# Performance work log

Hardware: AMD Instinct MI355X
Metric: run time of the kernel (lower is better)

The kernel has to match this reference:

```python
import jax, jax.numpy as jnp
import numpy as np

LEAK = 0.2

def _leaky(h):
    return jnp.where(h >= 0, h, LEAK * h)

def setup_inputs() -> dict:
    key = jax.random.key(0)
    ks = jax.random.split(key, 12)
    B, C, H, W = 4, 19, 256, 512
    ndf = 64
    dims = [C, ndf, ndf * 2, ndf * 4, ndf * 8, 1]  # 19->64->128->256->512->1
    inp = {
        "x": jax.random.normal(ks[0], (B, C, H, W), dtype=jnp.float32),
        "lbl": jax.random.uniform(ks[1], (B, H, W), dtype=jnp.float32),
    }
    for i in range(5):
        fan_in = dims[i]
        scale = 1.0 / np.sqrt(fan_in)
        inp[f"W{i+1}"] = jax.random.uniform(ks[2 + 2 * i], (dims[i + 1], dims[i]), minval=-scale, maxval=scale, dtype=jnp.float32)
        inp[f"b{i+1}"] = jax.random.uniform(ks[3 + 2 * i], (dims[i + 1],), minval=-scale, maxval=scale, dtype=jnp.float32)
    return inp

def reference(x, lbl, W1, b1, W2, b2, W3, b3, W4, b4, W5, b5):
    # x: [B, C, H, W] -> [B, H, W, C]; 1x1 convs == per-pixel linear layers
    h = jnp.transpose(x, (0, 2, 3, 1))
    h = _leaky(jnp.einsum('bhwc,oc->bhwo', h, W1) + b1)
    h = _leaky(jnp.einsum('bhwc,oc->bhwo', h, W2) + b2)
    h = _leaky(jnp.einsum('bhwc,oc->bhwo', h, W3) + b3)
    h = _leaky(jnp.einsum('bhwc,oc->bhwo', h, W4) + b4)
    z = (jnp.einsum('bhwc,oc->bhwo', h, W5) + b5)[..., 0]  # logits [B,H,W]
    # stable BCE-with-logits, mean over all elements; equals the per-pixel
    # mean-over-batch losses summed and divided by H*W as in the original loop
    bce = jnp.maximum(z, 0.0) - z * lbl + jnp.log1p(jnp.exp(-jnp.abs(z)))
    return jnp.mean(bce)
```

## Files before the change

### kernel.cpp

```cpp
#include <hip/hip_runtime.h>


#define HW_ 131072
#define NPIX 524288

using bf16x8 = __attribute__((ext_vector_type(8))) short;
using f32x4  = __attribute__((ext_vector_type(4))) float;

#define MFMA __builtin_amdgcn_mfma_f32_16x16x32_bf16

__device__ __forceinline__ unsigned short f2bf(float f) {
  unsigned u = __builtin_bit_cast(unsigned, f);
  u += 0x7FFFu + ((u >> 16) & 1u);
  return (unsigned short)(u >> 16);
}

__device__ __forceinline__ int kinv(int k) {
  return ((k >> 5) << 5) + (((k >> 2) & 1) << 4) + (((k >> 3) & 3) << 2) + (k & 3);
}

#define OW1 0
#define OW2 2048
#define OW3 10240
#define OW4 43008
#define WTOT 174080

template <int K0, int KP, bool PERM>
__device__ __forceinline__ void conv_layer(const float* __restrict__ W,
                                           unsigned short* __restrict__ out,
                                           int i) {
  int r9 = i & 511;
  int lane = r9 >> 3, j = r9 & 7;
  int frag = i >> 9;
  constexpr int KS = KP / 32;
  int ob = frag / KS, ks = frag - ob * KS;
  int o = ob * 16 + (lane & 15);
  int k = ks * 32 + ((lane >> 4) << 3) + j;
  int f = PERM ? kinv(k) : k;
  out[i] = f2bf(f < K0 ? W[o * K0 + f] : 0.f);
}

__global__ void wconv_kernel(const float* __restrict__ W1, const float* __restrict__ W2,
                             const float* __restrict__ W3, const float* __restrict__ W4,
                             unsigned short* __restrict__ wb) {
  int i = blockIdx.x * 256 + threadIdx.x;
  if (i < OW2) {
    conv_layer<19, 32, false>(W1, wb + OW1, i - OW1);
  } else if (i < OW3) {
    conv_layer<64, 64, true>(W2, wb + OW2, i - OW2);
  } else if (i < OW4) {
    conv_layer<128, 128, true>(W3, wb + OW3, i - OW3);
  } else if (i < WTOT) {
    conv_layer<256, 256, true>(W4, wb + OW4, i - OW4);
  }
}

__device__ __forceinline__ f32x4 leaky4(f32x4 v) {
  f32x4 r;
#pragma unroll
  for (int i = 0; i < 4; i++) r[i] = fmaxf(v[i], 0.2f * v[i]);
  return r;
}

__device__ __forceinline__ unsigned cvtpk(float lo, float hi) {
  unsigned r;
  asm("v_cvt_pk_bf16_f32 %0, %1, %2" : "=v"(r) : "v"(lo), "v"(hi));
  return r;
}
__device__ __forceinline__ bf16x8 pack8(f32x4 e, f32x4 o) {
  union { unsigned u[4]; bf16x8 v; } r;
  r.u[0] = cvtpk(e[0], e[1]);
  r.u[1] = cvtpk(e[2], e[3]);
  r.u[2] = cvtpk(o[0], o[1]);
  r.u[3] = cvtpk(o[2], o[3]);
  return r.v;
}

__device__ __forceinline__ void gl16(const unsigned char* g, unsigned char* l) {
  __builtin_amdgcn_global_load_lds(
      (const __attribute__((address_space(1))) unsigned int*)(const void*)g,
      (__attribute__((address_space(3))) unsigned int*)(void*)l, 16, 0, 0);
}
template <int NB>
__device__ __forceinline__ void stage(const unsigned char* __restrict__ g,
                                      unsigned char* l, int t) {
  int wbase = (t >> 6) << 10;
  int lbase = (t & 63) << 4;
#pragma unroll
  for (int i = 0; i < NB; i++)
    gl16(g + i * 4096 + wbase + lbase, l + i * 4096 + wbase);
}

#define LDF(bufp, lf) (*(const bf16x8*)((bufp) + ((lf) << 10) + (lane << 4)))

__global__ __launch_bounds__(256) __attribute__((amdgpu_waves_per_eu(2, 2)))
void disc_lds(const float* __restrict__ x, const float* __restrict__ lbl,
              const unsigned short* __restrict__ wb,
              const float* __restrict__ b1, const float* __restrict__ b2,
              const float* __restrict__ b3, const float* __restrict__ b4,
              const float* __restrict__ W5f, const float* __restrict__ b5,
              float* __restrict__ out) {
  __shared__ __align__(16) unsigned char sb0[32768];
  __shared__ __align__(16) unsigned char sb1[32768];

  int t = threadIdx.x;
  int wave = t >> 6, lane = t & 63;
  int g = lane >> 4, li = lane & 15;
  long px0 = ((long)blockIdx.x * 4 + wave) * 32;
  int b = (int)(px0 >> 17);
  int hw0 = (int)(px0 & (HW_ - 1));
  const unsigned char* wb8 = (const unsigned char*)wb;

  stage<5>(wb8, sb0, t);
  __syncthreads();

  stage<8>(wb8 + 20480, sb1, t);

  bf16x8 xb[2];
#pragma unroll
  for (int pb = 0; pb < 2; pb++) {
    const float* xp = x + (((long)b * 19) << 17) + hw0 + pb * 16 + li;
    bf16x8 v;
#pragma unroll
    for (int j = 0; j < 8; j++) {
      int c = 8 * g + j;
      float f = (c < 19) ? xp[(long)c << 17] : 0.f;
      v[j] = (short)f2bf(f);
    }
    xb[pb] = v;
  }

  bf16x8 h1[2][2];
#pragma unroll
  for (int obp = 0; obp < 2; obp++) {
    bf16x8 fE = LDF(sb0, 2 * obp);
    bf16x8 fO = LDF(sb0, 2 * obp + 1);
    f32x4 bE = *(const f32x4*)(b1 + 32 * obp + 4 * g);
    f32x4 bO = *(const f32x4*)(b1 + 32 * obp + 16 + 4 * g);
#pragma unroll
    for (int pb = 0; pb < 2; pb++) {
      f32x4 aE = MFMA(fE, xb[pb], bE, 0, 0, 0);
      f32x4 aO = MFMA(fO, xb[pb], bO, 0, 0, 0);
      h1[pb][obp] = pack8(leaky4(aE), leaky4(aO));
    }
  }

  bf16x8 h2[2][4];
#pragma unroll
  for (int obp = 0; obp < 4; obp++) {
    bf16x8 fE0 = LDF(sb0, 4 + 4 * obp);
    bf16x8 fE1 = LDF(sb0, 4 + 4 * obp + 1);
    bf16x8 fO0 = LDF(sb0, 4 + 4 * obp + 2);
    bf16x8 fO1 = LDF(sb0, 4 + 4 * obp + 3);
    f32x4 bE = *(const f32x4*)(b2 + 32 * obp + 4 * g);
    f32x4 bO = *(const f32x4*)(b2 + 32 * obp + 16 + 4 * g);
#pragma unroll
    for (int pb = 0; pb < 2; pb++) {
      f32x4 aE = MFMA(fE0, h1[pb][0], bE, 0, 0, 0);
      aE = MFMA(fE1, h1[pb][1], aE, 0, 0, 0);
      f32x4 aO = MFMA(fO0, h1[pb][0], bO, 0, 0, 0);
      aO = MFMA(fO1, h1[pb][1], aO, 0, 0, 0);
      h2[pb][obp] = pack8(leaky4(aE), leaky4(aO));
    }
  }
  __syncthreads();

  stage<8>(wb8 + 53248, sb0, t);

  bf16x8 h3[2][8];
#pragma unroll
  for (int obp = 0; obp < 4; obp++) {
    int lfE = (2 * obp) * 4, lfO = (2 * obp + 1) * 4;
    f32x4 bE = *(const f32x4*)(b3 + 32 * obp + 4 * g);
    f32x4 bO = *(const f32x4*)(b3 + 32 * obp + 16 + 4 * g);
    f32x4 aE[2], aO[2];
#pragma unroll
    for (int pb = 0; pb < 2; pb++) { aE[pb] = bE; aO[pb] = bO; }
#pragma unroll
    for (int ks = 0; ks < 4; ks++) {
      bf16x8 fE = LDF(sb1, lfE + ks);
      bf16x8 fO = LDF(sb1, lfO + ks);
#pragma unroll
      for (int pb = 0; pb < 2; pb++) {
        aE[pb] = MFMA(fE, h2[pb][ks], aE[pb], 0, 0, 0);
        aO[pb] = MFMA(fO, h2[pb][ks], aO[pb], 0, 0, 0);
      }
    }
#pragma unroll
    for (int pb = 0; pb < 2; pb++)
      h3[pb][obp] = pack8(leaky4(aE[pb]), leaky4(aO[pb]));
  }
  __syncthreads();

  stage<8>(wb8 + 86016, sb1, t);

#pragma unroll
  for (int obp = 4; obp < 8; obp++) {
    int lfE = (2 * obp) * 4 - 32, lfO = (2 * obp + 1) * 4 - 32;
    f32x4 bE = *(const f32x4*)(b3 + 32 * obp + 4 * g);
    f32x4 bO = *(const f32x4*)(b3 + 32 * obp + 16 + 4 * g);
    f32x4 aE[2], aO[2];
#pragma unroll
    for (int pb = 0; pb < 2; pb++) { aE[pb] = bE; aO[pb] = bO; }
#pragma unroll
    for (int ks = 0; ks < 4; ks++) {
      bf16x8 fE = LDF(sb0, lfE + ks);
      bf16x8 fO = LDF(sb0, lfO + ks);
#pragma unroll
      for (int pb = 0; pb < 2; pb++) {
        aE[pb] = MFMA(fE, h2[pb][ks], aE[pb], 0, 0, 0);
        aO[pb] = MFMA(fO, h2[pb][ks], aO[pb], 0, 0, 0);
      }
    }
#pragma unroll
    for (int pb = 0; pb < 2; pb++)
      h3[pb][obp] = pack8(leaky4(aE[pb]), leaky4(aO[pb]));
  }
  __syncthreads();

  f32x4 zp[2];
#pragma unroll
  for (int pb = 0; pb < 2; pb++) zp[pb] = f32x4{0.f, 0.f, 0.f, 0.f};

#pragma unroll 1
  for (int j = 0; j < 8; j++) {
    const unsigned char* cur = (j & 1) ? sb0 : sb1;
    unsigned char* nxt = (j & 1) ? sb1 : sb0;
    if (j < 7) stage<8>(wb8 + 86016 + (j + 1) * 32768, nxt, t);
    for (int oo = 0; oo < 4; oo++) {
      int ob = 4 * j + oo;
      f32x4 bv = *(const f32x4*)(b4 + 16 * ob + 4 * g);
      f32x4 w5v = *(const f32x4*)(W5f + 16 * ob + 4 * g);
      f32x4 a[2];
#pragma unroll
      for (int pb = 0; pb < 2; pb++) a[pb] = bv;
#pragma unroll
      for (int ks = 0; ks < 8; ks++) {
        bf16x8 f4 = LDF(cur, oo * 8 + ks);
#pragma unroll
        for (int pb = 0; pb < 2; pb++) a[pb] = MFMA(f4, h3[pb][ks], a[pb], 0, 0, 0);
      }
#pragma unroll
      for (int pb = 0; pb < 2; pb++) {
        f32x4 lv = leaky4(a[pb]);
#pragma unroll
        for (int i = 0; i < 4; i++) zp[pb][i] = fmaf(lv[i], w5v[i], zp[pb][i]);
      }
    }
    __syncthreads();
  }

  float zb[2];
#pragma unroll
  for (int pb = 0; pb < 2; pb++) {
    float s = zp[pb][0] + zp[pb][1] + zp[pb][2] + zp[pb][3];
    s += __shfl_xor(s, 16);
    s += __shfl_xor(s, 32);
    zb[pb] = s;
  }
  float w = 0.f;
  if (lane < 32) {
    float z = ((lane & 16) ? zb[1] : zb[0]) + b5[0];
    float lab = lbl[px0 + lane];
    w = fmaxf(z, 0.f) - z * lab + log1pf(expf(-fabsf(z)));
  }
#pragma unroll
  for (int m = 1; m <= 32; m <<= 1) w += __shfl_xor(w, m);
  float* zsp = (float*)sb0;
  if (lane == 0) zsp[wave] = w;
  __syncthreads();
  if (t == 0)
    atomicAdd(out, (zsp[0] + zsp[1] + zsp[2] + zsp[3]) * (1.f / (float)NPIX));
}

#define LDAG(dst, Wf, K0, KP, PERM, ob, ks)                                    \
  do {                                                                         \
    int o_ = (ob) * 16 + li;                                                   \
    for (int j_ = 0; j_ < 8; j_++) {                                           \
      int k_ = (ks) * 32 + (g << 3) + j_;                                      \
      int f_ = (PERM) ? kinv(k_) : k_;                                         \
      float v_ = f_ < (K0) ? (Wf)[o_ * (K0) + f_] : 0.f;                       \
      dst[j_] = (short)f2bf(v_);                                               \
    }                                                                          \
  } while (0)

__global__ __launch_bounds__(256, 1) void disc_fb(
    const float* __restrict__ x, const float* __restrict__ lbl,
    const float* __restrict__ W1f, const float* __restrict__ b1,
    const float* __restrict__ W2f, const float* __restrict__ b2,
    const float* __restrict__ W3f, const float* __restrict__ b3,
    const float* __restrict__ W4f, const float* __restrict__ b4,
    const float* __restrict__ W5f, const float* __restrict__ b5,
    float* __restrict__ out) {
  __shared__ float zs[4];
  int t = threadIdx.x;
  int wave = t >> 6, lane = t & 63;
  int g = lane >> 4, li = lane & 15;
  long px0 = ((long)blockIdx.x * 4 + wave) * 64;
  int b = (int)(px0 >> 17);
  int hw0 = (int)(px0 & (HW_ - 1));

  bf16x8 xb[4];
#pragma unroll
  for (int pb = 0; pb < 4; pb++) {
    const float* xp = x + (((long)b * 19) << 17) + hw0 + pb * 16 + li;
    bf16x8 v;
#pragma unroll
    for (int j = 0; j < 8; j++) {
      int c = 8 * g + j;
      float f = (c < 19) ? xp[(long)c << 17] : 0.f;
      v[j] = (short)f2bf(f);
    }
    xb[pb] = v;
  }

  bf16x8 h1[4][2];
#pragma unroll
  for (int obp = 0; obp < 2; obp++) {
    bf16x8 fE, fO;
    LDAG(fE, W1f, 19, 32, false, 2 * obp, 0);
    LDAG(fO, W1f, 19, 32, false, 2 * obp + 1, 0);
    f32x4 bE = *(const f32x4*)(b1 + 32 * obp + 4 * g);
    f32x4 bO = *(const f32x4*)(b1 + 32 * obp + 16 + 4 * g);
#pragma unroll
    for (int pb = 0; pb < 4; pb++) {
      f32x4 aE = MFMA(fE, xb[pb], bE, 0, 0, 0);
      f32x4 aO = MFMA(fO, xb[pb], bO, 0, 0, 0);
      h1[pb][obp] = pack8(leaky4(aE), leaky4(aO));
    }
  }

  bf16x8 h2[4][4];
#pragma unroll
  for (int obp = 0; obp < 4; obp++) {
    bf16x8 fE0, fE1, fO0, fO1;
    LDAG(fE0, W2f, 64, 64, true, 2 * obp, 0);
    LDAG(fE1, W2f, 64, 64, true, 2 * obp, 1);
    LDAG(fO0, W2f, 64, 64, true, 2 * obp + 1, 0);
    LDAG(fO1, W2f, 64, 64, true, 2 * obp + 1, 1);
    f32x4 bE = *(const f32x4*)(b2 + 32 * obp + 4 * g);
    f32x4 bO = *(const f32x4*)(b2 + 32 * obp + 16 + 4 * g);
#pragma unroll
    for (int pb = 0; pb < 4; pb++) {
      f32x4 aE = MFMA(fE0, h1[pb][0], bE, 0, 0, 0);
      aE = MFMA(fE1, h1[pb][1], aE, 0, 0, 0);
      f32x4 aO = MFMA(fO0, h1[pb][0], bO, 0, 0, 0);
      aO = MFMA(fO1, h1[pb][1], aO, 0, 0, 0);
      h2[pb][obp] = pack8(leaky4(aE), leaky4(aO));
    }
  }

  bf16x8 h3[4][8];
#pragma unroll
  for (int obp = 0; obp < 8; obp++) {
    f32x4 bE = *(const f32x4*)(b3 + 32 * obp + 4 * g);
    f32x4 bO = *(const f32x4*)(b3 + 32 * obp + 16 + 4 * g);
    f32x4 aE[4], aO[4];
#pragma unroll
    for (int pb = 0; pb < 4; pb++) { aE[pb] = bE; aO[pb] = bO; }
#pragma unroll
    for (int ks = 0; ks < 4; ks++) {
      bf16x8 fE, fO;
      LDAG(fE, W3f, 128, 128, true, 2 * obp, ks);
      LDAG(fO, W3f, 128, 128, true, 2 * obp + 1, ks);
#pragma unroll
      for (int pb = 0; pb < 4; pb++) {
        aE[pb] = MFMA(fE, h2[pb][ks], aE[pb], 0, 0, 0);
        aO[pb] = MFMA(fO, h2[pb][ks], aO[pb], 0, 0, 0);
      }
    }
#pragma unroll
    for (int pb = 0; pb < 4; pb++)
      h3[pb][obp] = pack8(leaky4(aE[pb]), leaky4(aO[pb]));
  }

  f32x4 zp[4];
#pragma unroll
  for (int pb = 0; pb < 4; pb++) zp[pb] = f32x4{0.f, 0.f, 0.f, 0.f};

  for (int ob = 0; ob < 32; ob++) {
    f32x4 bv = *(const f32x4*)(b4 + 16 * ob + 4 * g);
    f32x4 w5v = *(const f32x4*)(W5f + 16 * ob + 4 * g);
    f32x4 a[4];
#pragma unroll
    for (int pb = 0; pb < 4; pb++) a[pb] = bv;
#pragma unroll
    for (int ks = 0; ks < 8; ks++) {
      bf16x8 f4;
      LDAG(f4, W4f, 256, 256, true, ob, ks);
#pragma unroll
      for (int pb = 0; pb < 4; pb++) a[pb] = MFMA(f4, h3[pb][ks], a[pb], 0, 0, 0);
    }
#pragma unroll
    for (int pb = 0; pb < 4; pb++) {
      f32x4 lv = leaky4(a[pb]);
#pragma unroll
      for (int i = 0; i < 4; i++) zp[pb][i] = fmaf(lv[i], w5v[i], zp[pb][i]);
    }
  }

  float zb[4];
#pragma unroll
  for (int pb = 0; pb < 4; pb++) {
    float s = zp[pb][0] + zp[pb][1] + zp[pb][2] + zp[pb][3];
    s += __shfl_xor(s, 16);
    s += __shfl_xor(s, 32);
    zb[pb] = s;
  }
  float zsel = (g == 0) ? zb[0] : (g == 1) ? zb[1] : (g == 2) ? zb[2] : zb[3];
  float z = zsel + b5[0];
  float lab = lbl[px0 + lane];
  float w = fmaxf(z, 0.f) - z * lab + log1pf(expf(-fabsf(z)));
#pragma unroll
  for (int m = 1; m <= 32; m <<= 1) w += __shfl_xor(w, m);
  if (lane == 0) zs[wave] = w;
  __syncthreads();
  if (t == 0)
    atomicAdd(out, (zs[0] + zs[1] + zs[2] + zs[3]) * (1.f / (float)NPIX));
}

extern "C" void kernel_launch(void* const* d_in, const int* in_sizes, int n_in,
                              void* d_out, int out_size, void* d_ws, size_t ws_size,
                              hipStream_t stream) {
  const float* x   = (const float*)d_in[0];
  const float* lbl = (const float*)d_in[1];
  const float* W1  = (const float*)d_in[2];
  const float* b1  = (const float*)d_in[3];
  const float* W2  = (const float*)d_in[4];
  const float* b2  = (const float*)d_in[5];
  const float* W3  = (const float*)d_in[6];
  const float* b3  = (const float*)d_in[7];
  const float* W4  = (const float*)d_in[8];
  const float* b4  = (const float*)d_in[9];
  const float* W5  = (const float*)d_in[10];
  const float* b5  = (const float*)d_in[11];
  float* out = (float*)d_out;

  hipMemsetAsync(d_out, 0, sizeof(float), stream);

  bool pre = ws_size >= (size_t)WTOT * sizeof(unsigned short);
  if (pre) {
    unsigned short* wbp = (unsigned short*)d_ws;
    wconv_kernel<<<(WTOT + 255) / 256, 256, 0, stream>>>(W1, W2, W3, W4, wbp);
    disc_lds<<<NPIX / 128, 256, 0, stream>>>(x, lbl, wbp, b1, b2, b3, b4, W5, b5, out);
  } else {
    disc_fb<<<NPIX / 256, 256, 0, stream>>>(x, lbl, W1, b1, W2, b2, W3, b3, W4, b4,
                                            W5, b5, out);
  }
}
```

Measured before the change: 191.0 us.

## Double workgroup size to 8 waves so each staged weight tile serves more pixels

```diff
diff --git a/kernel.cpp b/kernel.cpp
--- a/kernel.cpp
+++ b/kernel.cpp
@@ -81,19 +81,19 @@
       (const __attribute__((address_space(1))) unsigned int*)(const void*)g,
       (__attribute__((address_space(3))) unsigned int*)(void*)l, 16, 0, 0);
 }
-template <int NB>
+template <int NSEG>
 __device__ __forceinline__ void stage(const unsigned char* __restrict__ g,
-                                      unsigned char* l, int t) {
-  int wbase = (t >> 6) << 10;
-  int lbase = (t & 63) << 4;
-#pragma unroll
-  for (int i = 0; i < NB; i++)
-    gl16(g + i * 4096 + wbase + lbase, l + i * 4096 + wbase);
+                                      unsigned char* l, int wave, int lane) {
+#pragma unroll
+  for (int i = 0; i * 8 < NSEG; i++) {
+    int s = wave + i * 8;
+    if (s < NSEG) gl16(g + (s << 10) + (lane << 4), l + (s << 10));
+  }
 }
 
 #define LDF(bufp, lf) (*(const bf16x8*)((bufp) + ((lf) << 10) + (lane << 4)))
 
-__global__ __launch_bounds__(256) __attribute__((amdgpu_waves_per_eu(2, 2)))
+__global__ __launch_bounds__(512) __attribute__((amdgpu_waves_per_eu(4, 4)))
 void disc_lds(const float* __restrict__ x, const float* __restrict__ lbl,
               const unsigned short* __restrict__ wb,
               const float* __restrict__ b1, const float* __restrict__ b2,
@@ -106,15 +106,15 @@
   int t = threadIdx.x;
   int wave = t >> 6, lane = t & 63;
   int g = lane >> 4, li = lane & 15;
-  long px0 = ((long)blockIdx.x * 4 + wave) * 32;
+  long px0 = ((long)blockIdx.x * 8 + wave) * 32;
   int b = (int)(px0 >> 17);
   int hw0 = (int)(px0 & (HW_ - 1));
   const unsigned char* wb8 = (const unsigned char*)wb;
 
-  stage<5>(wb8, sb0, t);
-  __syncthreads();
-
-  stage<8>(wb8 + 20480, sb1, t);
+  stage<20>(wb8, sb0, wave, lane);
+  __syncthreads();
+
+  stage<32>(wb8 + 20480, sb1, wave, lane);
 
   bf16x8 xb[2];
 #pragma unroll
@@ -165,7 +165,7 @@
   }
   __syncthreads();
 
-  stage<8>(wb8 + 53248, sb0, t);
+  stage<32>(wb8 + 53248, sb0, wave, lane);
 
   bf16x8 h3[2][8];
 #pragma unroll
@@ -192,7 +192,7 @@
   }
   __syncthreads();
 
-  stage<8>(wb8 + 86016, sb1, t);
+  stage<32>(wb8 + 86016, sb1, wave, lane);
 
 #pragma unroll
   for (int obp = 4; obp < 8; obp++) {
@@ -226,7 +226,7 @@
   for (int j = 0; j < 8; j++) {
     const unsigned char* cur = (j & 1) ? sb0 : sb1;
     unsigned char* nxt = (j & 1) ? sb1 : sb0;
-    if (j < 7) stage<8>(wb8 + 86016 + (j + 1) * 32768, nxt, t);
+    if (j < 7) stage<32>(wb8 + 86016 + (j + 1) * 32768, nxt, wave, lane);
     for (int oo = 0; oo < 4; oo++) {
       int ob = 4 * j + oo;
       f32x4 bv = *(const f32x4*)(b4 + 16 * ob + 4 * g);
@@ -269,8 +269,12 @@
   float* zsp = (float*)sb0;
   if (lane == 0) zsp[wave] = w;
   __syncthreads();
-  if (t == 0)
-    atomicAdd(out, (zsp[0] + zsp[1] + zsp[2] + zsp[3]) * (1.f / (float)NPIX));
+  if (t == 0) {
+    float s = 0.f;
+#pragma unroll
+    for (int i = 0; i < 8; i++) s += zsp[i];
+    atomicAdd(out, s * (1.f / (float)NPIX));
+  }
 }
 
 #define LDAG(dst, Wf, K0, KP, PERM, ob, ks)                                    \
@@ -442,7 +446,7 @@
   if (pre) {
     unsigned short* wbp = (unsigned short*)d_ws;
     wconv_kernel<<<(WTOT + 255) / 256, 256, 0, stream>>>(W1, W2, W3, W4, wbp);
-    disc_lds<<<NPIX / 128, 256, 0, stream>>>(x, lbl, wbp, b1, b2, b3, b4, W5, b5, out);
+    disc_lds<<<NPIX / 256, 512, 0, stream>>>(x, lbl, wbp, b1, b2, b3, b4, W5, b5, out);
   } else {
     disc_fb<<<NPIX / 256, 256, 0, stream>>>(x, lbl, W1, b1, W2, b2, W3, b3, W4, b4,
                                             W5, b5, out);
```

Result: slower. 469.1 us (+145.6%).

## Shrink LDS staging buffers to 24KB to raise occupancy to three waves

Applied to the files above, without the earlier changes.

```diff
diff --git a/kernel.cpp b/kernel.cpp
--- a/kernel.cpp
+++ b/kernel.cpp
@@ -81,27 +81,24 @@
       (const __attribute__((address_space(1))) unsigned int*)(const void*)g,
       (__attribute__((address_space(3))) unsigned int*)(void*)l, 16, 0, 0);
 }
-template <int NB>
-__device__ __forceinline__ void stage(const unsigned char* __restrict__ g,
-                                      unsigned char* l, int t) {
-  int wbase = (t >> 6) << 10;
-  int lbase = (t & 63) << 4;
-#pragma unroll
-  for (int i = 0; i < NB; i++)
-    gl16(g + i * 4096 + wbase + lbase, l + i * 4096 + wbase);
+__device__ __forceinline__ void stage_n(const unsigned char* __restrict__ g,
+                                        unsigned char* l, int nseg,
+                                        int wave, int lane) {
+  for (int s = wave; s < nseg; s += 4)
+    gl16(g + (s << 10) + (lane << 4), l + (s << 10));
 }
 
 #define LDF(bufp, lf) (*(const bf16x8*)((bufp) + ((lf) << 10) + (lane << 4)))
 
-__global__ __launch_bounds__(256) __attribute__((amdgpu_waves_per_eu(2, 2)))
+__global__ __launch_bounds__(256) __attribute__((amdgpu_waves_per_eu(3, 3)))
 void disc_lds(const float* __restrict__ x, const float* __restrict__ lbl,
               const unsigned short* __restrict__ wb,
               const float* __restrict__ b1, const float* __restrict__ b2,
               const float* __restrict__ b3, const float* __restrict__ b4,
               const float* __restrict__ W5f, const float* __restrict__ b5,
               float* __restrict__ out) {
-  __shared__ __align__(16) unsigned char sb0[32768];
-  __shared__ __align__(16) unsigned char sb1[32768];
+  __shared__ __align__(16) unsigned char sb0[24576];
+  __shared__ __align__(16) unsigned char sb1[24576];
 
   int t = threadIdx.x;
   int wave = t >> 6, lane = t & 63;
@@ -111,10 +108,10 @@
   int hw0 = (int)(px0 & (HW_ - 1));
   const unsigned char* wb8 = (const unsigned char*)wb;
 
-  stage<5>(wb8, sb0, t);
-  __syncthreads();
-
-  stage<8>(wb8 + 20480, sb1, t);
+  stage_n(wb8, sb0, 20, wave, lane);
+  __syncthreads();
+
+  stage_n(wb8 + 20480, sb1, 24, wave, lane);
 
   bf16x8 xb[2];
 #pragma unroll
@@ -165,12 +162,12 @@
   }
   __syncthreads();
 
-  stage<8>(wb8 + 53248, sb0, t);
-
   bf16x8 h3[2][8];
-#pragma unroll
-  for (int obp = 0; obp < 4; obp++) {
-    int lfE = (2 * obp) * 4, lfO = (2 * obp + 1) * 4;
+  stage_n(wb8 + 45056, sb0, 24, wave, lane);
+#pragma unroll
+  for (int ol = 0; ol < 3; ol++) {
+    int obp = ol;
+    int lfE = ol * 8, lfO = ol * 8 + 4;
     f32x4 bE = *(const f32x4*)(b3 + 32 * obp + 4 * g);
     f32x4 bO = *(const f32x4*)(b3 + 32 * obp + 16 + 4 * g);
     f32x4 aE[2], aO[2];
@@ -192,11 +189,11 @@
   }
   __syncthreads();
 
-  stage<8>(wb8 + 86016, sb1, t);
-
-#pragma unroll
-  for (int obp = 4; obp < 8; obp++) {
-    int lfE = (2 * obp) * 4 - 32, lfO = (2 * obp + 1) * 4 - 32;
+  stage_n(wb8 + 69632, sb1, 16, wave, lane);
+#pragma unroll
+  for (int ol = 0; ol < 3; ol++) {
+    int obp = 3 + ol;
+    int lfE = ol * 8, lfO = ol * 8 + 4;
     f32x4 bE = *(const f32x4*)(b3 + 32 * obp + 4 * g);
     f32x4 bO = *(const f32x4*)(b3 + 32 * obp + 16 + 4 * g);
     f32x4 aE[2], aO[2];
@@ -218,17 +215,47 @@
   }
   __syncthreads();
 
+  stage_n(wb8 + 86016, sb0, 24, wave, lane);
+#pragma unroll
+  for (int ol = 0; ol < 2; ol++) {
+    int obp = 6 + ol;
+    int lfE = ol * 8, lfO = ol * 8 + 4;
+    f32x4 bE = *(const f32x4*)(b3 + 32 * obp + 4 * g);
+    f32x4 bO = *(const f32x4*)(b3 + 32 * obp + 16 + 4 * g);
+    f32x4 aE[2], aO[2];
+#pragma unroll
+    for (int pb = 0; pb < 2; pb++) { aE[pb] = bE; aO[pb] = bO; }
+#pragma unroll
+    for (int ks = 0; ks < 4; ks++) {
+      bf16x8 fE = LDF(sb1, lfE + ks);
+      bf16x8 fO = LDF(sb1, lfO + ks);
+#pragma unroll
+      for (int pb = 0; pb < 2; pb++) {
+        aE[pb] = MFMA(fE, h2[pb][ks], aE[pb], 0, 0, 0);
+        aO[pb] = MFMA(fO, h2[pb][ks], aO[pb], 0, 0, 0);
+      }
+    }
+#pragma unroll
+    for (int pb = 0; pb < 2; pb++)
+      h3[pb][obp] = pack8(leaky4(aE[pb]), leaky4(aO[pb]));
+  }
+  __syncthreads();
+
   f32x4 zp[2];
 #pragma unroll
   for (int pb = 0; pb < 2; pb++) zp[pb] = f32x4{0.f, 0.f, 0.f, 0.f};
 
 #pragma unroll 1
-  for (int j = 0; j < 8; j++) {
-    const unsigned char* cur = (j & 1) ? sb0 : sb1;
-    unsigned char* nxt = (j & 1) ? sb1 : sb0;
-    if (j < 7) stage<8>(wb8 + 86016 + (j + 1) * 32768, nxt, t);
-    for (int oo = 0; oo < 4; oo++) {
-      int ob = 4 * j + oo;
+  for (int j = 0; j < 11; j++) {
+    const unsigned char* cur = (j & 1) ? sb1 : sb0;
+    unsigned char* nxt = (j & 1) ? sb0 : sb1;
+    if (j < 10) {
+      int nseg = (j < 9) ? 24 : 16;
+      stage_n(wb8 + 86016 + (j + 1) * 24576, nxt, nseg, wave, lane);
+    }
+    int nobs = (j < 10) ? 3 : 2;
+    for (int oo = 0; oo < nobs; oo++) {
+      int ob = 3 * j + oo;
       f32x4 bv = *(const f32x4*)(b4 + 16 * ob + 4 * g);
       f32x4 w5v = *(const f32x4*)(W5f + 16 * ob + 4 * g);
       f32x4 a[2];
```

After: 191.1 us. No clear change (+0.0%).

## Triple-buffer weight staging in 16KB chunks with vmcnt waits and raise occupancy

Applied to the files above, without the earlier changes.

```diff
diff --git a/kernel.cpp b/kernel.cpp
--- a/kernel.cpp
+++ b/kernel.cpp
@@ -6,8 +6,13 @@
 
 using bf16x8 = __attribute__((ext_vector_type(8))) short;
 using f32x4  = __attribute__((ext_vector_type(4))) float;
+using f32x2  = __attribute__((ext_vector_type(2))) float;
 
 #define MFMA __builtin_amdgcn_mfma_f32_16x16x32_bf16
+#define VMCNT4 asm volatile("s_waitcnt vmcnt(4)" ::: "memory")
+#define VMCNT0 asm volatile("s_waitcnt vmcnt(0)" ::: "memory")
+#define BAR __builtin_amdgcn_s_barrier()
+#define SCHED0 __builtin_amdgcn_sched_barrier(0)
 
 __device__ __forceinline__ unsigned short f2bf(float f) {
   unsigned u = __builtin_bit_cast(unsigned, f);
@@ -55,10 +60,26 @@
   }
 }
 
+__device__ __forceinline__ f32x2 pk_mul(f32x2 a, f32x2 b) {
+  f32x2 d;
+  asm("v_pk_mul_f32 %0, %1, %2" : "=v"(d) : "v"(a), "v"(b));
+  return d;
+}
+__device__ __forceinline__ f32x2 pk_fma(f32x2 a, f32x2 b, f32x2 c) {
+  f32x2 d;
+  asm("v_pk_fma_f32 %0, %1, %2, %3" : "=v"(d) : "v"(a), "v"(b), "v"(c));
+  return d;
+}
+
 __device__ __forceinline__ f32x4 leaky4(f32x4 v) {
+  f32x2 c = {0.2f, 0.2f};
+  f32x2 lo = {v[0], v[1]}, hi = {v[2], v[3]};
+  f32x2 ml = pk_mul(lo, c), mh = pk_mul(hi, c);
   f32x4 r;
-#pragma unroll
-  for (int i = 0; i < 4; i++) r[i] = fmaxf(v[i], 0.2f * v[i]);
+  r[0] = fmaxf(v[0], ml[0]);
+  r[1] = fmaxf(v[1], ml[1]);
+  r[2] = fmaxf(v[2], mh[0]);
+  r[3] = fmaxf(v[3], mh[1]);
   return r;
 }
 
@@ -81,27 +102,25 @@
       (const __attribute__((address_space(1))) unsigned int*)(const void*)g,
       (__attribute__((address_space(3))) unsigned int*)(void*)l, 16, 0, 0);
 }
-template <int NB>
-__device__ __forceinline__ void stage(const unsigned char* __restrict__ g,
-                                      unsigned char* l, int t) {
-  int wbase = (t >> 6) << 10;
-  int lbase = (t & 63) << 4;
-#pragma unroll
-  for (int i = 0; i < NB; i++)
-    gl16(g + i * 4096 + wbase + lbase, l + i * 4096 + wbase);
+__device__ __forceinline__ void stage16(const unsigned char* __restrict__ g,
+                                        unsigned char* l, int wave, int lane) {
+#pragma unroll
+  for (int i = 0; i < 4; i++) {
+    int s = wave + 4 * i;
+    gl16(g + (s << 10) + (lane << 4), l + (s << 10));
+  }
 }
 
 #define LDF(bufp, lf) (*(const bf16x8*)((bufp) + ((lf) << 10) + (lane << 4)))
 
-__global__ __launch_bounds__(256) __attribute__((amdgpu_waves_per_eu(2, 2)))
+__global__ __launch_bounds__(256) __attribute__((amdgpu_waves_per_eu(3, 3)))
 void disc_lds(const float* __restrict__ x, const float* __restrict__ lbl,
               const unsigned short* __restrict__ wb,
               const float* __restrict__ b1, const float* __restrict__ b2,
               const float* __restrict__ b3, const float* __restrict__ b4,
               const float* __restrict__ W5f, const float* __restrict__ b5,
               float* __restrict__ out) {
-  __shared__ __align__(16) unsigned char sb0[32768];
-  __shared__ __align__(16) unsigned char sb1[32768];
+  __shared__ __align__(16) unsigned char sb[49152];
 
   int t = threadIdx.x;
   int wave = t >> 6, lane = t & 63;
@@ -111,10 +130,10 @@
   int hw0 = (int)(px0 & (HW_ - 1));
   const unsigned char* wb8 = (const unsigned char*)wb;
 
-  stage<5>(wb8, sb0, t);
-  __syncthreads();
-
-  stage<8>(wb8 + 20480, sb1, t);
+  bf16x8 fW1[4];
+#pragma unroll
+  for (int f = 0; f < 4; f++)
+    fW1[f] = *(const bf16x8*)(wb8 + (f << 10) + (lane << 4));
 
   bf16x8 xb[2];
 #pragma unroll
@@ -130,105 +149,102 @@
     xb[pb] = v;
   }
 
+  stage16(wb8 + 4096, sb, wave, lane);
+  stage16(wb8 + 20480, sb + 16384, wave, lane);
+
   bf16x8 h1[2][2];
 #pragma unroll
   for (int obp = 0; obp < 2; obp++) {
-    bf16x8 fE = LDF(sb0, 2 * obp);
-    bf16x8 fO = LDF(sb0, 2 * obp + 1);
     f32x4 bE = *(const f32x4*)(b1 + 32 * obp + 4 * g);
     f32x4 bO = *(const f32x4*)(b1 + 32 * obp + 16 + 4 * g);
+    f32x4 aE[2], aO[2];
 #pragma unroll
     for (int pb = 0; pb < 2; pb++) {
-      f32x4 aE = MFMA(fE, xb[pb], bE, 0, 0, 0);
-      f32x4 aO = MFMA(fO, xb[pb], bO, 0, 0, 0);
-      h1[pb][obp] = pack8(leaky4(aE), leaky4(aO));
-    }
-  }
-
+      aE[pb] = MFMA(fW1[2 * obp], xb[pb], bE, 0, 0, 0);
+      aO[pb] = MFMA(fW1[2 * obp + 1], xb[pb], bO, 0, 0, 0);
+    }
+#pragma unroll
+    for (int pb = 0; pb < 2; pb++)
+      h1[pb][obp] = pack8(leaky4(aE[pb]), leaky4(aO[pb]));
+  }
+
+  VMCNT4; BAR; SCHED0;
+  stage16(wb8 + 36864, sb + 32768, wave, lane);
   bf16x8 h2[2][4];
-#pragma unroll
-  for (int obp = 0; obp < 4; obp++) {
-    bf16x8 fE0 = LDF(sb0, 4 + 4 * obp);
-    bf16x8 fE1 = LDF(sb0, 4 + 4 * obp + 1);
-    bf16x8 fO0 = LDF(sb0, 4 + 4 * obp + 2);
-    bf16x8 fO1 = LDF(sb0, 4 + 4 * obp + 3);
-    f32x4 bE = *(const f32x4*)(b2 + 32 * obp + 4 * g);
-    f32x4 bO = *(const f32x4*)(b2 + 32 * obp + 16 + 4 * g);
-#pragma unroll
-    for (int pb = 0; pb < 2; pb++) {
-      f32x4 aE = MFMA(fE0, h1[pb][0], bE, 0, 0, 0);
-      aE = MFMA(fE1, h1[pb][1], aE, 0, 0, 0);
-      f32x4 aO = MFMA(fO0, h1[pb][0], bO, 0, 0, 0);
-      aO = MFMA(fO1, h1[pb][1], aO, 0, 0, 0);
-      h2[pb][obp] = pack8(leaky4(aE), leaky4(aO));
-    }
-  }
-  __syncthreads();
-
-  stage<8>(wb8 + 53248, sb0, t);
+  {
+    const unsigned char* cur = sb;
+#pragma unroll
+    for (int obp = 0; obp < 4; obp++) {
+      bf16x8 fE0 = LDF(cur, 4 * obp);
+      bf16x8 fE1 = LDF(cur, 4 * obp + 1);
+      bf16x8 fO0 = LDF(cur, 4 * obp + 2);
+      bf16x8 fO1 = LDF(cur, 4 * obp + 3);
+      f32x4 bE = *(const f32x4*)(b2 + 32 * obp + 4 * g);
+      f32x4 bO = *(const f32x4*)(b2 + 32 * obp + 16 + 4 * g);
+      f32x4 aE[2], aO[2];
+#pragma unroll
+      for (int pb = 0; pb < 2; pb++) {
+        aE[pb] = MFMA(fE0, h1[pb][0], bE, 0, 0, 0);
+        aE[pb] = MFMA(fE1, h1[pb][1], aE[pb], 0, 0, 0);
+        aO[pb] = MFMA(fO0, h1[pb][0], bO, 0, 0, 0);
+        aO[pb] = MFMA(fO1, h1[pb][1], aO[pb], 0, 0, 0);
+      }
+#pragma unroll
+      for (int pb = 0; pb < 2; pb++)
+        h2[pb][obp] = pack8(leaky4(aE[pb]), leaky4(aO[pb]));
+    }
+  }
 
   bf16x8 h3[2][8];
 #pragma unroll
-  for (int obp = 0; obp < 4; obp++) {
-    int lfE = (2 * obp) * 4, lfO = (2 * obp + 1) * 4;
-    f32x4 bE = *(const f32x4*)(b3 + 32 * obp + 4 * g);
-    f32x4 bO = *(const f32x4*)(b3 + 32 * obp + 16 + 4 * g);
-    f32x4 aE[2], aO[2];
-#pragma unroll
-    for (int pb = 0; pb < 2; pb++) { aE[pb] = bE; aO[pb] = bO; }
-#pragma unroll
-    for (int ks = 0; ks < 4; ks++) {
-      bf16x8 fE = LDF(sb1, lfE + ks);
-      bf16x8 fO = LDF(sb1, lfO + ks);
-#pragma unroll
-      for (int pb = 0; pb < 2; pb++) {
-        aE[pb] = MFMA(fE, h2[pb][ks], aE[pb], 0, 0, 0);
-        aO[pb] = MFMA(fO, h2[pb][ks], aO[pb], 0, 0, 0);
+  for (int k = 0; k < 4; k++) {
+    int c = 1 + k;
+    VMCNT4; BAR; SCHED0;
+    int cc = c + 2;
+    const unsigned char* src = (cc <= 4) ? (wb8 + 20480 + ((cc - 1) << 14))
+                                         : (wb8 + 86016 + ((cc - 5) << 14));
+    stage16(src, sb + ((cc % 3) << 14), wave, lane);
+    const unsigned char* cur = sb + ((c % 3) << 14);
+#pragma unroll
+    for (int o = 0; o < 2; o++) {
+      int obp = 2 * k + o;
+      f32x4 bE = *(const f32x4*)(b3 + 32 * obp + 4 * g);
+      f32x4 bO = *(const f32x4*)(b3 + 32 * obp + 16 + 4 * g);
+      f32x4 aE[2], aO[2];
+#pragma unroll
+      for (int pb = 0; pb < 2; pb++) { aE[pb] = bE; aO[pb] = bO; }
+#pragma unroll
+      for (int ks = 0; ks < 4; ks++) {
+        bf16x8 fE = LDF(cur, o * 8 + ks);
+        bf16x8 fO = LDF(cur, o * 8 + 4 + ks);
+#pragma unroll
+        for (int pb = 0; pb < 2; pb++) {
+          aE[pb] = MFMA(fE, h2[pb][ks], aE[pb], 0, 0, 0);
+          aO[pb] = MFMA(fO, h2[pb][ks], aO[pb], 0, 0, 0);
+        }
       }
-    }
-#pragma unroll
-    for (int pb = 0; pb < 2; pb++)
-      h3[pb][obp] = pack8(leaky4(aE[pb]), leaky4(aO[pb]));
-  }
-  __syncthreads();
-
-  stage<8>(wb8 + 86016, sb1, t);
-
-#pragma unroll
-  for (int obp = 4; obp < 8; obp++) {
-    int lfE = (2 * obp) * 4 - 32, lfO = (2 * obp + 1) * 4 - 32;
-    f32x4 bE = *(const f32x4*)(b3 + 32 * obp + 4 * g);
-    f32x4 bO = *(const f32x4*)(b3 + 32 * obp + 16 + 4 * g);
-    f32x4 aE[2], aO[2];
-#pragma unroll
-    for (int pb = 0; pb < 2; pb++) { aE[pb] = bE; aO[pb] = bO; }
-#pragma unroll
-    for (int ks = 0; ks < 4; ks++) {
-      bf16x8 fE = LDF(sb0, lfE + ks);
-      bf16x8 fO = LDF(sb0, lfO + ks);
-#pragma unroll
-      for (int pb = 0; pb < 2; pb++) {
-        aE[pb] = MFMA(fE, h2[pb][ks], aE[pb], 0, 0, 0);
-        aO[pb] = MFMA(fO, h2[pb][ks], aO[pb], 0, 0, 0);
-      }
-    }
-#pragma unroll
-    for (int pb = 0; pb < 2; pb++)
-      h3[pb][obp] = pack8(leaky4(aE[pb]), leaky4(aO[pb]));
-  }
-  __syncthreads();
+#pragma unroll
+      for (int pb = 0; pb < 2; pb++)
+        h3[pb][obp] = pack8(leaky4(aE[pb]), leaky4(aO[pb]));
+    }
+  }
 
   f32x4 zp[2];
 #pragma unroll
   for (int pb = 0; pb < 2; pb++) zp[pb] = f32x4{0.f, 0.f, 0.f, 0.f};
 
 #pragma unroll 1
-  for (int j = 0; j < 8; j++) {
-    const unsigned char* cur = (j & 1) ? sb0 : sb1;
-    unsigned char* nxt = (j & 1) ? sb1 : sb0;
-    if (j < 7) stage<8>(wb8 + 86016 + (j + 1) * 32768, nxt, t);
-    for (int oo = 0; oo < 4; oo++) {
-      int ob = 4 * j + oo;
+  for (int c = 5; c <= 20; c++) {
+    if (c == 20) { VMCNT0; } else { VMCNT4; }
+    BAR; SCHED0;
+    if (c + 2 <= 20)
+      stage16(wb8 + 86016 + ((c - 3) << 14), sb + (((c + 2) % 3) << 14),
+              wave, lane);
+    const unsigned char* cur = sb + ((c % 3) << 14);
+    int ob0 = 2 * (c - 5);
+#pragma unroll
+    for (int oo = 0; oo < 2; oo++) {
+      int ob = ob0 + oo;
       f32x4 bv = *(const f32x4*)(b4 + 16 * ob + 4 * g);
       f32x4 w5v = *(const f32x4*)(W5f + 16 * ob + 4 * g);
       f32x4 a[2];
@@ -243,11 +259,13 @@
 #pragma unroll
       for (int pb = 0; pb < 2; pb++) {
         f32x4 lv = leaky4(a[pb]);
-#pragma unroll
-        for (int i = 0; i < 4; i++) zp[pb][i] = fmaf(lv[i], w5v[i], zp[pb][i]);
+        f32x2 zlo = {zp[pb][0], zp[pb][1]}, zhi = {zp[pb][2], zp[pb][3]};
+        zlo = pk_fma(f32x2{lv[0], lv[1]}, f32x2{w5v[0], w5v[1]}, zlo);
+        zhi = pk_fma(f32x2{lv[2], lv[3]}, f32x2{w5v[2], w5v[3]}, zhi);
+        zp[pb][0] = zlo[0]; zp[pb][1] = zlo[1];
+        zp[pb][2] = zhi[0]; zp[pb][3] = zhi[1];
       }
     }
-    __syncthreads();
   }
 
   float zb[2];
@@ -266,7 +284,7 @@
   }
 #pragma unroll
   for (int m = 1; m <= 32; m <<= 1) w += __shfl_xor(w, m);
-  float* zsp = (float*)sb0;
+  float* zsp = (float*)sb;
   if (lane == 0) zsp[wave] = w;
   __syncthreads();
   if (t == 0)
@@ -436,7 +454,7 @@
   const float* b5  = (const float*)d_in[11];
   float* out = (float*)d_out;
 
-  hipMemsetAsync(d_out, 0, sizeof(float), stream);
+  (void)hipMemsetAsync(d_out, 0, sizeof(float), stream);
 
   bool pre = ws_size >= (size_t)WTOT * sizeof(unsigned short);
   if (pre) {
```

Result: slower. 196.6 us (+2.9%).
